# Optimization experiments

Measured on AMD Instinct MI355X. Metric: run time of the kernel, lower is better.

Reference implementation:

```python
import jax, jax.numpy as jnp
import numpy as np

B, S, D, N, NC = 2, 1024, 1024, 8192, 8


def _srw_chunked(x, h, emb_norm, tau_offset, w_read, w_write, n_chunks):
    Bd, Sd, Dd = x.shape
    Nd = emb_norm.shape[0]
    cs = Nd // n_chunks
    h_bf = h.astype(jnp.bfloat16)
    x_bf = x.astype(jnp.bfloat16)
    emb_bf = emb_norm.astype(jnp.bfloat16)
    read_bf = w_read.astype(jnp.bfloat16)
    write_bf = w_write.astype(jnp.bfloat16)
    z1 = jnp.zeros((Bd, Sd, 1))

    @jax.checkpoint
    def estimate_stats(h, emb, nc_val):
        ec0 = jax.lax.dynamic_slice_in_dim(emb, 0, cs, axis=0)
        sc0 = h @ ec0.T
        s_sum = sc0.sum(axis=-1, keepdims=True).astype(jnp.float32) * nc_val
        sq_sum = (sc0 ** 2).sum(axis=-1, keepdims=True).astype(jnp.float32) * nc_val
        return (s_sum, sq_sum)

    s_sum, sq_sum = estimate_stats(h_bf, emb_bf, n_chunks)
    s_mean = s_sum / Nd
    s_std = jnp.sqrt(sq_sum / Nd - s_mean ** 2) + 1e-08
    tau = s_mean + tau_offset * s_std
    tau_bf = tau.astype(jnp.bfloat16)

    @jax.checkpoint
    def gsrw_step(carry, i):
        out, es, em, ac, lbs, lbq = carry
        s = i * cs
        ec = jax.lax.dynamic_slice_in_dim(emb_bf, s, cs, axis=0)
        rc = jax.lax.dynamic_slice_in_dim(read_bf, s, cs, axis=0)
        wc = jax.lax.dynamic_slice_in_dim(write_bf, s, cs, axis=0)
        sc = h_bf @ ec.T  # [B,S,cs]
        raw = sc - tau_bf
        gc = jnp.where(raw > 0, raw, (1e-06 * jnp.exp(jnp.clip(raw.astype(jnp.float32), -10.0, 0.0))).astype(jnp.bfloat16))
        gc = jnp.clip(gc, 0.0, 10.0)
        eg = (jnp.exp(gc.astype(jnp.float32)) - 1.0).astype(jnp.bfloat16)
        ef = eg.astype(jnp.float32)
        xr = x_bf @ rc.T  # [B,S,cs]
        co = ((eg * xr) @ wc).astype(jnp.float32)  # [B,S,D]
        gn = ef.mean(axis=(0, 1))
        lbs = lbs + gn.sum()
        lbq = lbq + (gn ** 2).sum()
        return ((out + co,
                 es + ef.sum(axis=-1, keepdims=True),
                 jnp.maximum(em, ef.max(axis=-1, keepdims=True)),
                 ac + (raw > 0).sum(axis=-1, keepdims=True).astype(jnp.float32),
                 lbs, lbq), None)

    z_scalar = jnp.float32(0.0)
    init = (jnp.zeros((Bd, Sd, Dd), dtype=jnp.float32), z1,
            jnp.full((Bd, Sd, 1), -1000000000.0), z1, z_scalar, z_scalar)
    (raw_out, tes, tem, tac, lb_sum, lb_sq), _ = jax.lax.scan(gsrw_step, init, jnp.arange(n_chunks))
    inv_es = (1.0 / (tes + 1e-08)).astype(jnp.bfloat16)
    gs = jnp.tanh(tem).astype(jnp.bfloat16)
    out = raw_out * inv_es * gs
    exp_sum_scalar = tes.mean() + 1e-08
    norm_lb_sum = lb_sum / exp_sum_scalar
    norm_lb_sq = lb_sq / exp_sum_scalar ** 2
    lb_loss = norm_lb_sq * Nd - 2.0 * norm_lb_sum + 1.0
    gs_mean = jnp.tanh(tem).mean()
    es_mean = tes.mean()
    return (out.astype(jnp.float32), tac / Nd, tem, lb_loss, gs_mean, es_mean)


def setup_inputs() -> dict:
    key = jax.random.key(0)
    k = jax.random.split(key, 6)
    x = jax.random.normal(k[0], (B, S, D), jnp.float32)
    h = jax.random.normal(k[1], (B, S, D), jnp.float32)
    emb = jax.random.normal(k[2], (N, D), jnp.float32) * 0.02
    w_read = jax.random.normal(k[3], (N, D), jnp.float32) * 0.02
    w_write = jax.random.normal(k[4], (N, D), jnp.float32) * 0.02
    tau_offset = jax.random.normal(k[5], (B, S, 1), jnp.float32) * 0.1
    return {"x": x, "h": h, "emb": emb, "tau_offset": tau_offset,
            "w_read": w_read, "w_write": w_write, "n_chunks": NC}


def reference(x, h, emb, tau_offset, w_read, w_write, n_chunks):
    # caller (_know_forward) unit-normalizes the embedding pool first
    emb_norm = emb / (jnp.linalg.norm(emb, axis=-1, keepdims=True) + 1e-08)
    out, active_frac, gate_max, lb_loss, gs_mean, es_mean = _srw_chunked(
        x, h, emb_norm, tau_offset, w_read, w_write, n_chunks)
    return out
```

## Files before the change

### kernel.cpp

```cpp
#include <hip/hip_runtime.h>


#define MDIM 2048
#define DDIM 1024
#define NDIM 8192

typedef __attribute__((ext_vector_type(8))) __bf16 bf16x8;
typedef __attribute__((ext_vector_type(4))) float f32x4;

static __device__ __forceinline__ unsigned short f2b(float f) {
  unsigned u = __float_as_uint(f);
  u = (u + 0x7FFFu + ((u >> 16) & 1u)) >> 16;
  return (unsigned short)u;
}
static __device__ __forceinline__ float b2f(unsigned short s) {
  return __uint_as_float(((unsigned)s) << 16);
}

#define LDSF(off) (*(const bf16x8*)(lds + (off)))
#define MFMA_BF16 __builtin_amdgcn_mfma_f32_16x16x32_bf16

static __device__ __forceinline__ void stage_half(const unsigned short* __restrict__ src,
                                                  int ld, int row0, int k0,
                                                  char* lds, int lds_off, int w, int l) {
  const int rsub = l >> 3;
  const int col = k0 + 8 * ((l & 7) ^ rsub);
#pragma unroll
  for (int j = 0; j < 2; ++j) {
    const unsigned short* g =
        src + (size_t)(row0 + w * 8 + j * 64 + rsub) * (size_t)ld + col;
    __builtin_amdgcn_global_load_lds(
        (const __attribute__((address_space(1))) unsigned int*)(const void*)g,
        (__attribute__((address_space(3))) unsigned int*)(void*)(lds + lds_off + j * 8192 + w * 1024),
        16, 0, 0);
  }
}

template <int PAR, bool SA, bool SB, int VMC>
static __device__ __forceinline__ void ktile(const unsigned short* __restrict__ asrc,
                                             const unsigned short* __restrict__ bsrc,
                                             int ld, int m0, int n0, int kA, int kB,
                                             char* lds, f32x4 (&acc)[8][4],
                                             int w, int l, int wr, int wc,
                                             int arow_off, int brow_off, int kx0, int kx1) {
  const int ab = PAR * 65536 + wr * 16384;
  const int bb = PAR * 65536 + 32768 + (wc >> 1) * 16384;
  const int nxt = (1 - PAR) * 65536;
  bf16x8 a[4][2], blo[2][2], bhi[2][2];
  if (SA) stage_half(asrc, ld, m0, kA, lds, nxt, w, l);
#pragma unroll
  for (int m = 0; m < 4; ++m) {
    a[m][0] = LDSF(ab + arow_off + m * 2048 + kx0);
    a[m][1] = LDSF(ab + arow_off + m * 2048 + kx1);
  }
#pragma unroll
  for (int n = 0; n < 2; ++n) {
    blo[n][0] = LDSF(bb + brow_off + n * 2048 + kx0);
    blo[n][1] = LDSF(bb + brow_off + n * 2048 + kx1);
  }
  asm volatile("s_waitcnt lgkmcnt(8)" ::: "memory");
  __builtin_amdgcn_s_barrier();
  asm volatile("s_waitcnt lgkmcnt(0)" ::: "memory");
  __builtin_amdgcn_s_setprio(1);
#pragma unroll
  for (int ks = 0; ks < 2; ++ks)
#pragma unroll
    for (int n = 0; n < 2; ++n)
#pragma unroll
      for (int m = 0; m < 4; ++m)
        acc[m][n] = MFMA_BF16(a[m][ks], blo[n][ks], acc[m][n], 0, 0, 0);
  __builtin_amdgcn_s_setprio(0);
  __builtin_amdgcn_s_barrier();
  if (SA) stage_half(asrc, ld, m0 + 128, kA, lds, nxt + 16384, w, l);
#pragma unroll
  for (int n = 0; n < 2; ++n) {
    bhi[n][0] = LDSF(bb + brow_off + (n + 2) * 2048 + kx0);
    bhi[n][1] = LDSF(bb + brow_off + (n + 2) * 2048 + kx1);
  }
  __builtin_amdgcn_s_barrier();
  asm volatile("s_waitcnt lgkmcnt(0)" ::: "memory");
  __builtin_amdgcn_s_setprio(1);
#pragma unroll
  for (int ks = 0; ks < 2; ++ks)
#pragma unroll
    for (int n = 0; n < 2; ++n)
#pragma unroll
      for (int m = 0; m < 4; ++m)
        acc[m][n + 2] = MFMA_BF16(a[m][ks], bhi[n][ks], acc[m][n + 2], 0, 0, 0);
  __builtin_amdgcn_s_setprio(0);
  __builtin_amdgcn_s_barrier();
  if (SB) stage_half(bsrc, ld, n0, kB, lds, PAR * 65536 + 32768, w, l);
#pragma unroll
  for (int m = 0; m < 4; ++m) {
    a[m][0] = LDSF(ab + arow_off + (m + 4) * 2048 + kx0);
    a[m][1] = LDSF(ab + arow_off + (m + 4) * 2048 + kx1);
  }
  __builtin_amdgcn_s_barrier();
  asm volatile("s_waitcnt lgkmcnt(0)" ::: "memory");
  __builtin_amdgcn_s_setprio(1);
#pragma unroll
  for (int ks = 0; ks < 2; ++ks)
#pragma unroll
    for (int n = 0; n < 2; ++n)
#pragma unroll
      for (int m = 0; m < 4; ++m)
        acc[m + 4][n + 2] = MFMA_BF16(a[m][ks], bhi[n][ks], acc[m + 4][n + 2], 0, 0, 0);
  __builtin_amdgcn_s_setprio(0);
  __builtin_amdgcn_s_barrier();
  if (SB) stage_half(bsrc, ld, n0 + 128, kB, lds, PAR * 65536 + 49152, w, l);
  __builtin_amdgcn_s_setprio(1);
#pragma unroll
  for (int ks = 0; ks < 2; ++ks)
#pragma unroll
    for (int n = 0; n < 2; ++n)
#pragma unroll
      for (int m = 0; m < 4; ++m)
        acc[m + 4][n] = MFMA_BF16(a[m][ks], blo[n][ks], acc[m + 4][n], 0, 0, 0);
  __builtin_amdgcn_s_setprio(0);
  if (VMC == 4) asm volatile("s_waitcnt vmcnt(4)" ::: "memory");
  if (VMC == 0) asm volatile("s_waitcnt vmcnt(0)" ::: "memory");
  __builtin_amdgcn_s_barrier();
}

static __device__ __forceinline__ void gemm256(const unsigned short* __restrict__ asrc,
                                               const unsigned short* __restrict__ bsrc,
                                               int ld, int m0, int n0, int kbase,
                                               char* lds, f32x4 (&acc)[8][4],
                                               int w, int l, int wr, int wc) {
  const int lrow = l & 15, lk = l >> 4;
  const int axor = (l & 7) << 4;
  const int kx0 = (lk << 4) ^ axor;
  const int kx1 = (64 | (lk << 4)) ^ axor;
  const int arow_off = lrow * 128;
  const int brow_off = ((wc & 1) * 64 + lrow) * 128;

  stage_half(asrc, ld, m0,       kbase,      lds, 0,             w, l);
  stage_half(asrc, ld, m0 + 128, kbase,      lds, 16384,         w, l);
  stage_half(bsrc, ld, n0,       kbase,      lds, 32768,         w, l);
  stage_half(bsrc, ld, n0 + 128, kbase,      lds, 49152,         w, l);
  stage_half(bsrc, ld, n0,       kbase + 64, lds, 65536 + 32768, w, l);
  stage_half(bsrc, ld, n0 + 128, kbase + 64, lds, 65536 + 49152, w, l);
  asm volatile("s_waitcnt vmcnt(4)" ::: "memory");
  __builtin_amdgcn_s_barrier();

#pragma unroll 1
  for (int s = 0; s < 14; s += 2) {
    ktile<0, true, true, 4>(asrc, bsrc, ld, m0, n0, kbase + (s + 1) * 64,
                            kbase + (s + 2) * 64, lds, acc, w, l, wr, wc,
                            arow_off, brow_off, kx0, kx1);
    ktile<1, true, true, 4>(asrc, bsrc, ld, m0, n0, kbase + (s + 2) * 64,
                            kbase + (s + 3) * 64, lds, acc, w, l, wr, wc,
                            arow_off, brow_off, kx0, kx1);
  }
  ktile<0, true, false, 0>(asrc, bsrc, ld, m0, n0, kbase + 15 * 64, 0, lds, acc,
                           w, l, wr, wc, arow_off, brow_off, kx0, kx1);
  ktile<1, false, false, -1>(asrc, bsrc, ld, m0, n0, 0, 0, lds, acc,
                             w, l, wr, wc, arow_off, brow_off, kx0, kx1);
}


__global__ __launch_bounds__(256) void k_prep(const float* __restrict__ emb,
                                              const float* __restrict__ w_read,
                                              const float* __restrict__ h,
                                              const float* __restrict__ x,
                                              const float* __restrict__ w_write,
                                              unsigned short* __restrict__ eb,
                                              unsigned short* __restrict__ rb,
                                              unsigned short* __restrict__ hb,
                                              unsigned short* __restrict__ xb,
                                              unsigned short* __restrict__ wbT) {
  const int b = blockIdx.x, t = threadIdx.x;
  if (b < 8192) {
    const float4 v = ((const float4*)(emb + (size_t)b * 1024))[t];
    float ss = v.x * v.x + v.y * v.y + v.z * v.z + v.w * v.w;
#pragma unroll
    for (int off = 1; off < 64; off <<= 1) ss += __shfl_xor(ss, off, 64);
    __shared__ float wsum[4];
    if ((t & 63) == 0) wsum[t >> 6] = ss;
    __syncthreads();
    const float denom = sqrtf(wsum[0] + wsum[1] + wsum[2] + wsum[3]) + 1e-8f;
    ushort4 o;
    o.x = f2b(v.x / denom);
    o.y = f2b(v.y / denom);
    o.z = f2b(v.z / denom);
    o.w = f2b(v.w / denom);
    ((ushort4*)(eb + (size_t)b * 1024))[t] = o;
  } else if (b < 20480) {
    const float* src;
    unsigned short* dst;
    int i;
    if (b < 16384) { src = w_read; dst = rb; i = (b - 8192) * 256 + t; }
    else if (b < 18432) { src = h; dst = hb; i = (b - 16384) * 256 + t; }
    else { src = x; dst = xb; i = (b - 18432) * 256 + t; }
    const float4 v = ((const float4*)src)[i];
    ushort4 o;
    o.x = f2b(v.x);
    o.y = f2b(v.y);
    o.z = f2b(v.z);
    o.w = f2b(v.w);
    ((ushort4*)dst)[i] = o;
  } else {
    __shared__ float tsm[64][65];
    const int b2 = b - 20480;
    const int nb = b2 & 127, db = b2 >> 7;
    const int r = t >> 2, c4 = (t & 3) * 16;
#pragma unroll
    for (int j = 0; j < 4; ++j) {
      const float4 v = *(const float4*)&w_write[(size_t)(nb * 64 + r) * 1024 + db * 64 + c4 + 4 * j];
      tsm[r][c4 + 4 * j + 0] = v.x;
      tsm[r][c4 + 4 * j + 1] = v.y;
      tsm[r][c4 + 4 * j + 2] = v.z;
      tsm[r][c4 + 4 * j + 3] = v.w;
    }
    __syncthreads();
    const int dr = t >> 2, nc0 = (t & 3) * 16;
    unsigned pk[8];
#pragma unroll
    for (int j = 0; j < 8; ++j) {
      const unsigned lo = f2b(tsm[nc0 + 2 * j][dr]);
      const unsigned hi = f2b(tsm[nc0 + 2 * j + 1][dr]);
      pk[j] = lo | (hi << 16);
    }
    uint4* dst = (uint4*)(wbT + (size_t)(db * 64 + dr) * 8192 + nb * 64 + nc0);
    uint4 w0, w1;
    w0.x = pk[0]; w0.y = pk[1]; w0.z = pk[2]; w0.w = pk[3];
    w1.x = pk[4]; w1.y = pk[5]; w1.z = pk[6]; w1.w = pk[7];
    dst[0] = w0;
    dst[1] = w1;
  }
}


template <int TROWS>
static __device__ __forceinline__ void stage_tile(const unsigned short* __restrict__ src,
                                                  int row0, int k0, int ld,
                                                  unsigned short* lds, int wave, int lane) {
  const int rsub = lane >> 3;
  const int csub = (lane & 7) << 3;
#pragma unroll
  for (int q = 0; q < TROWS / 32; ++q) {
    const int p = q * 4 + wave;
    const unsigned short* g =
        src + (size_t)(row0 + p * 8 + rsub) * (size_t)ld + (size_t)(k0 + csub);
    __builtin_amdgcn_global_load_lds(
        (const __attribute__((address_space(1))) unsigned int*)(const void*)g,
        (__attribute__((address_space(3))) unsigned int*)(void*)(lds + p * 512),
        16, 0, 0);
  }
}

__global__ __launch_bounds__(256, 2) void k_stats(const unsigned short* __restrict__ hb,
                                                  const unsigned short* __restrict__ eb,
                                                  float* __restrict__ stat_s,
                                                  float* __restrict__ stat_q) {
  __shared__ unsigned short a_sm[128 * 64];
  __shared__ unsigned short b_sm[128 * 64];
  __shared__ float red_s[2][128];
  __shared__ float red_q[2][128];
  const int t = threadIdx.x;
  const int wave = t >> 6, lane = t & 63;
  const int wr = wave >> 1, wc = wave & 1;
  const int m0 = blockIdx.x * 128, n0 = blockIdx.y * 128;
  const int arow = lane & 15;
  const int kcol = (lane >> 4) << 3;
  f32x4 acc[4][4];
#pragma unroll
  for (int m = 0; m < 4; ++m)
#pragma unroll
    for (int n = 0; n < 4; ++n) acc[m][n] = (f32x4)0.0f;
  for (int k0 = 0; k0 < 1024; k0 += 64) {
    stage_tile<128>(hb, m0, k0, 1024, a_sm, wave, lane);
    stage_tile<128>(eb, n0, k0, 1024, b_sm, wave, lane);
    asm volatile("s_waitcnt vmcnt(0)" ::: "memory");
    __syncthreads();
#pragma unroll
    for (int ks = 0; ks < 2; ++ks) {
      bf16x8 af[4], bfr[4];
#pragma unroll
      for (int m = 0; m < 4; ++m)
        af[m] = *(const bf16x8*)&a_sm[(wr * 64 + m * 16 + arow) * 64 + ks * 32 + kcol];
#pragma unroll
      for (int n = 0; n < 4; ++n)
        bfr[n] = *(const bf16x8*)&b_sm[(wc * 64 + n * 16 + arow) * 64 + ks * 32 + kcol];
#pragma unroll
      for (int m = 0; m < 4; ++m)
#pragma unroll
        for (int n = 0; n < 4; ++n)
          acc[m][n] = MFMA_BF16(af[m], bfr[n], acc[m][n], 0, 0, 0);
    }
    __syncthreads();
  }

  float s_r[4][4], q_r[4][4];
#pragma unroll
  for (int m = 0; m < 4; ++m)
#pragma unroll
    for (int i = 0; i < 4; ++i) { s_r[m][i] = 0.f; q_r[m][i] = 0.f; }
#pragma unroll
  for (int m = 0; m < 4; ++m)
#pragma unroll
    for (int n = 0; n < 4; ++n)
#pragma unroll
      for (int i = 0; i < 4; ++i) {
        const float scf = b2f(f2b(acc[m][n][i]));
        s_r[m][i] += scf;
        q_r[m][i] += b2f(f2b(scf * scf));
      }
#pragma unroll
  for (int m = 0; m < 4; ++m)
#pragma unroll
    for (int i = 0; i < 4; ++i) {
      float s = s_r[m][i], q = q_r[m][i];
      for (int off = 1; off < 16; off <<= 1) {
        s += __shfl_xor(s, off, 64);
        q += __shfl_xor(q, off, 64);
      }
      if ((lane & 15) == 0) {
        const int rloc = wr * 64 + m * 16 + (lane >> 4) * 4 + i;
        red_s[wc][rloc] = s;
        red_q[wc][rloc] = q;
      }
    }
  __syncthreads();
  if (t < 128) {
    stat_s[(size_t)(m0 + t) * 8 + blockIdx.y] = red_s[0][t] + red_s[1][t];
    stat_q[(size_t)(m0 + t) * 8 + blockIdx.y] = red_q[0][t] + red_q[1][t];
  }
}

__global__ void k_tau(const float* __restrict__ stat_s, const float* __restrict__ stat_q,
                      const float* __restrict__ tau_off, float* __restrict__ tau) {
  const int r = blockIdx.x * 256 + threadIdx.x;
  if (r >= MDIM) return;
  float S = 0.f, Q = 0.f;
#pragma unroll
  for (int j = 0; j < 8; ++j) {
    S += stat_s[(size_t)r * 8 + j];
    Q += stat_q[(size_t)r * 8 + j];
  }
  const float s_sum = S * 8.0f;
  const float sq_sum = Q * 8.0f;
  const float mean = s_sum * (1.0f / 8192.0f);
  const float var = __fsub_rn(sq_sum * (1.0f / 8192.0f), __fmul_rn(mean, mean));
  const float sd = __fadd_rn(__fsqrt_rn(var), 1e-8f);
  const float tv = __fadd_rn(mean, __fmul_rn(tau_off[r], sd));
  tau[r] = b2f(f2b(tv));
}


__global__ __launch_bounds__(512, 2) void k_gate(const unsigned short* __restrict__ hb,
                                                 const unsigned short* __restrict__ eb,
                                                 const unsigned short* __restrict__ xb,
                                                 const unsigned short* __restrict__ rb,
                                                 const float* __restrict__ tau,
                                                 unsigned short* __restrict__ Aeg,
                                                 float* __restrict__ es_part,
                                                 float* __restrict__ em_part) {
  __shared__ __align__(16) char lds[131072];
  const int t = threadIdx.x, w = t >> 6, l = t & 63;
  const int wr = w >> 2, wc = w & 3;
  const int bid = blockIdx.x;
  const int swz = (bid & 7) * 32 + (bid >> 3);
  const int m0 = (swz >> 5) * 256, n0 = (swz & 31) * 256;
  const int lrow = l & 15, lk = l >> 4;

  f32x4 acc[8][4];
#pragma unroll
  for (int m = 0; m < 8; ++m)
#pragma unroll
    for (int n = 0; n < 4; ++n) acc[m][n] = (f32x4)0.0f;
  gemm256(hb, eb, 1024, m0, n0, 0, lds, acc, w, l, wr, wc);

  __syncthreads();
  float* tau_sm = (float*)lds;
  float* red_es = (float*)(lds + 1024);
  float* red_em = (float*)(lds + 1024 + 4096);
  if (t < 256) tau_sm[t] = tau[m0 + t];
  __syncthreads();
#pragma unroll
  for (int m = 0; m < 8; ++m) {
#pragma unroll
    for (int i = 0; i < 4; ++i) {
      const int rl = wr * 128 + m * 16 + lk * 4 + i;
      const float taub = tau_sm[rl];
      float es_v = 0.f, em_v = 0.f;
#pragma unroll
      for (int n = 0; n < 4; ++n) {
        const float scf = b2f(f2b(acc[m][n][i]));
        const float rawf = b2f(f2b(scf - taub));
        float gcf;
        if (rawf > 0.f) gcf = fminf(rawf, 10.0f);
        else gcf = b2f(f2b(1e-6f * expf(fmaxf(rawf, -10.0f))));
        const unsigned short egu = f2b(expf(gcf) - 1.0f);
        const float ef = b2f(egu);
        es_v += ef;
        em_v = fmaxf(em_v, ef);
        Aeg[(size_t)(m0 + rl) * NDIM + (size_t)(n0 + wc * 64 + n * 16 + lrow)] = egu;
      }
      for (int off = 1; off < 16; off <<= 1) {
        es_v += __shfl_xor(es_v, off, 64);
        em_v = fmaxf(em_v, __shfl_xor(em_v, off, 64));
      }
      if (lrow == 0) {
        red_es[wc * 256 + rl] = es_v;
        red_em[wc * 256 + rl] = em_v;
      }
    }
  }
  __syncthreads();
  if (t < 256) {
    const float s = red_es[t] + red_es[256 + t] + red_es[512 + t] + red_es[768 + t];
    const float e = fmaxf(fmaxf(red_em[t], red_em[256 + t]),
                          fmaxf(red_em[512 + t], red_em[768 + t]));
    es_part[(size_t)(m0 + t) * 32 + (n0 >> 8)] = s;
    em_part[(size_t)(m0 + t) * 32 + (n0 >> 8)] = e;
  }
  __syncthreads();

#pragma unroll
  for (int m = 0; m < 8; ++m)
#pragma unroll
    for (int n = 0; n < 4; ++n) acc[m][n] = (f32x4)0.0f;
  gemm256(xb, rb, 1024, m0, n0, 0, lds, acc, w, l, wr, wc);

#pragma unroll
  for (int m = 0; m < 8; ++m)
#pragma unroll
    for (int n = 0; n < 4; ++n)
#pragma unroll
      for (int i = 0; i < 4; ++i) {
        const int rl = wr * 128 + m * 16 + lk * 4 + i;
        const size_t idx =
            (size_t)(m0 + rl) * NDIM + (size_t)(n0 + wc * 64 + n * 16 + lrow);
        const unsigned short egu = Aeg[idx];
        const float xrf = b2f(f2b(acc[m][n][i]));
        Aeg[idx] = f2b(b2f(egu) * xrf);
      }
}


__global__ __launch_bounds__(512, 2) void k_out(const unsigned short* __restrict__ A,
                                                const unsigned short* __restrict__ wbT,
                                                unsigned short* __restrict__ pacc) {
  __shared__ __align__(16) char lds[131072];
  const int t = threadIdx.x, w = t >> 6, l = t & 63;
  const int wr = w >> 2, wc = w & 3;
  const int bid = blockIdx.x;
  const int swz = (bid & 7) * 32 + (bid >> 3);
  const int bm = swz >> 5, chunk = (swz >> 2) & 7, bd = swz & 3;
  const int m0 = bm * 256, d0 = bd * 256;
  f32x4 acc[8][4];
#pragma unroll
  for (int m = 0; m < 8; ++m)
#pragma unroll
    for (int n = 0; n < 4; ++n) acc[m][n] = (f32x4)0.0f;
  gemm256(A, wbT, 8192, m0, d0, chunk * 1024, lds, acc, w, l, wr, wc);

  const int lrow = l & 15, lk = l >> 4;
#pragma unroll
  for (int m = 0; m < 8; ++m)
#pragma unroll
    for (int n = 0; n < 4; ++n)
#pragma unroll
      for (int i = 0; i < 4; ++i) {
        const int rl = wr * 128 + m * 16 + lk * 4 + i;
        pacc[((size_t)chunk * MDIM + (m0 + rl)) * DDIM +
             (size_t)(d0 + wc * 64 + n * 16 + lrow)] = f2b(acc[m][n][i]);
      }
}


__global__ void k_scale(const float* __restrict__ es_part, const float* __restrict__ em_part,
                        float* __restrict__ scale2) {
  const int r = blockIdx.x * 256 + threadIdx.x;
  if (r >= MDIM) return;
  float s = 0.f, m = 0.f;
#pragma unroll
  for (int j = 0; j < 32; ++j) {
    s += es_part[(size_t)r * 32 + j];
    m = fmaxf(m, em_part[(size_t)r * 32 + j]);
  }
  scale2[2 * r] = b2f(f2b(1.0f / (s + 1e-8f)));
  scale2[2 * r + 1] = b2f(f2b(tanhf(m)));
}

__global__ __launch_bounds__(256) void k_finish(const unsigned short* __restrict__ pacc,
                                                const float* __restrict__ scale2,
                                                float* __restrict__ outp) {
  const int t = blockIdx.x * 256 + threadIdx.x;
  const int r = t >> 8;
  const int d4 = (t & 255) * 4;
  float sx = 0.f, sy = 0.f, sz = 0.f, sw = 0.f;
#pragma unroll
  for (int c = 0; c < 8; ++c) {
    const ushort4 v = *(const ushort4*)(pacc + ((size_t)c * MDIM + r) * DDIM + d4);
    sx += b2f(v.x);
    sy += b2f(v.y);
    sz += b2f(v.z);
    sw += b2f(v.w);
  }
  const float inv = scale2[2 * r];
  const float gsv = scale2[2 * r + 1];
  float4 o;
  o.x = (sx * inv) * gsv;
  o.y = (sy * inv) * gsv;
  o.z = (sz * inv) * gsv;
  o.w = (sw * inv) * gsv;
  *(float4*)(outp + (size_t)r * DDIM + d4) = o;
}


extern "C" void kernel_launch(void* const* d_in, const int* in_sizes, int n_in,
                              void* d_out, int out_size, void* d_ws, size_t ws_size,
                              hipStream_t stream) {
  const float* x = (const float*)d_in[0];
  const float* h = (const float*)d_in[1];
  const float* emb = (const float*)d_in[2];
  const float* tau_off = (const float*)d_in[3];
  const float* w_read = (const float*)d_in[4];
  const float* w_write = (const float*)d_in[5];

  char* ws = (char*)d_ws;
  const size_t MB = 1024 * 1024;
  unsigned short* rb = (unsigned short*)(ws);
  unsigned short* eb = (unsigned short*)(ws + 16 * MB);
  unsigned short* wbT = (unsigned short*)(ws + 32 * MB);
  unsigned short* hb = (unsigned short*)(ws + 48 * MB);
  unsigned short* xb = (unsigned short*)(ws + 52 * MB);
  unsigned short* Aeg = (unsigned short*)(ws + 56 * MB);
  unsigned short* pacc = (unsigned short*)(ws);
  float* tau = (float*)(ws + 88 * MB);
  float* stat_s = (float*)(ws + 88 * MB + 1 * 65536);
  float* stat_q = (float*)(ws + 88 * MB + 2 * 65536);
  float* es_part = (float*)(ws + 88 * MB + 3 * 65536);
  float* em_part = (float*)(ws + 88 * MB + 7 * 65536);
  float* scale2 = (float*)(ws + 88 * MB + 11 * 65536);
  if (ws_size < 88 * MB + 12 * 65536) return;
  float* outp = (float*)d_out;

  k_prep<<<22528, 256, 0, stream>>>(emb, w_read, h, x, w_write, eb, rb, hb, xb, wbT);
  k_stats<<<dim3(MDIM / 128, 8), 256, 0, stream>>>(hb, eb, stat_s, stat_q);
  k_tau<<<MDIM / 256, 256, 0, stream>>>(stat_s, stat_q, tau_off, tau);
  k_gate<<<256, 512, 0, stream>>>(hb, eb, xb, rb, tau, Aeg, es_part, em_part);
  k_scale<<<MDIM / 256, 256, 0, stream>>>(es_part, em_part, scale2);
  k_out<<<256, 512, 0, stream>>>(Aeg, wbT, pacc);
  k_finish<<<(MDIM * DDIM / 4) / 256, 256, 0, stream>>>(pacc, scale2, outp);
}
```

Before: 224.9 us.

## Restructure GEMM k-loop to prefetch next-tile fragments and reorder block mapping

The 256x256 GEMM inner tile is rescheduled so A and B register fragments for the next k-step are read from LDS while the current MFMAs run. Fragments are carried across tiles, and both A and B halves are preloaded two stages deep in the prologue. Block-to-tile mapping in the gate and output kernels is changed so blocks on the same XCD share N-columns or chunks, aiming for better L2 reuse. The prep kernel reorders its block ranges so the transpose blocks run first. This adds register pressure and a more delicate barrier and waitcnt ordering.

After: 424.6 us. 1.89x slower.

```diff
diff --git a/kernel.cpp b/kernel.cpp
--- a/kernel.cpp
+++ b/kernel.cpp
@@ -36,89 +36,108 @@
   }
 }
 
-template <int PAR, bool SA, bool SB, int VMC>
+template <int PAR, bool STG, bool RD, int VM>
 static __device__ __forceinline__ void ktile(const unsigned short* __restrict__ asrc,
                                              const unsigned short* __restrict__ bsrc,
-                                             int ld, int m0, int n0, int kA, int kB,
+                                             int ld, int m0, int n0, int kS,
                                              char* lds, f32x4 (&acc)[8][4],
+                                             bf16x8 (&aLO)[4][2], bf16x8 (&aHI)[4][2],
+                                             bf16x8 (&bLO)[2][2], bf16x8 (&bHI)[2][2],
                                              int w, int l, int wr, int wc,
                                              int arow_off, int brow_off, int kx0, int kx1) {
   const int ab = PAR * 65536 + wr * 16384;
   const int bb = PAR * 65536 + 32768 + (wc >> 1) * 16384;
-  const int nxt = (1 - PAR) * 65536;
-  bf16x8 a[4][2], blo[2][2], bhi[2][2];
-  if (SA) stage_half(asrc, ld, m0, kA, lds, nxt, w, l);
+  const int abn = (1 - PAR) * 65536 + wr * 16384;
+  const int bbn = (1 - PAR) * 65536 + 32768 + (wc >> 1) * 16384;
+
+#pragma unroll
+  for (int n = 0; n < 2; ++n) {
+    bHI[n][0] = LDSF(bb + brow_off + (n + 2) * 2048 + kx0);
+    bHI[n][1] = LDSF(bb + brow_off + (n + 2) * 2048 + kx1);
+  }
+  __builtin_amdgcn_s_barrier();
+  __builtin_amdgcn_s_setprio(1);
+#pragma unroll
+  for (int ks = 0; ks < 2; ++ks)
+#pragma unroll
+    for (int n = 0; n < 2; ++n)
+#pragma unroll
+      for (int m = 0; m < 4; ++m)
+        acc[m][n] = MFMA_BF16(aLO[m][ks], bLO[n][ks], acc[m][n], 0, 0, 0);
+  __builtin_amdgcn_s_setprio(0);
+  asm volatile("s_waitcnt lgkmcnt(0)" ::: "memory");
+  __builtin_amdgcn_s_barrier();
+
+  if (STG) {
+    stage_half(bsrc, ld, n0, kS, lds, PAR * 65536 + 32768, w, l);
+    stage_half(bsrc, ld, n0 + 128, kS, lds, PAR * 65536 + 49152, w, l);
+  }
 #pragma unroll
   for (int m = 0; m < 4; ++m) {
-    a[m][0] = LDSF(ab + arow_off + m * 2048 + kx0);
-    a[m][1] = LDSF(ab + arow_off + m * 2048 + kx1);
-  }
+    aHI[m][0] = LDSF(ab + arow_off + (m + 4) * 2048 + kx0);
+    aHI[m][1] = LDSF(ab + arow_off + (m + 4) * 2048 + kx1);
+  }
+  if (VM == 4) asm volatile("s_waitcnt vmcnt(4)" ::: "memory");
+  if (VM == 0) asm volatile("s_waitcnt vmcnt(0)" ::: "memory");
+  __builtin_amdgcn_s_barrier();
+  __builtin_amdgcn_s_setprio(1);
+#pragma unroll
+  for (int ks = 0; ks < 2; ++ks)
+#pragma unroll
+    for (int n = 0; n < 2; ++n)
+#pragma unroll
+      for (int m = 0; m < 4; ++m)
+        acc[m][n + 2] = MFMA_BF16(aLO[m][ks], bHI[n][ks], acc[m][n + 2], 0, 0, 0);
+  __builtin_amdgcn_s_setprio(0);
+  asm volatile("s_waitcnt lgkmcnt(0)" ::: "memory");
+  __builtin_amdgcn_s_barrier();
+
+  if (STG) stage_half(asrc, ld, m0, kS, lds, PAR * 65536, w, l);
+  if (RD) {
+#pragma unroll
+    for (int m = 0; m < 4; ++m) {
+      aLO[m][0] = LDSF(abn + arow_off + m * 2048 + kx0);
+      aLO[m][1] = LDSF(abn + arow_off + m * 2048 + kx1);
+    }
+  }
+  __builtin_amdgcn_s_barrier();
+  __builtin_amdgcn_s_setprio(1);
+#pragma unroll
+  for (int ks = 0; ks < 2; ++ks)
+#pragma unroll
+    for (int n = 0; n < 2; ++n)
+#pragma unroll
+      for (int m = 0; m < 4; ++m)
+        acc[m + 4][n + 2] = MFMA_BF16(aHI[m][ks], bHI[n][ks], acc[m + 4][n + 2], 0, 0, 0);
+  __builtin_amdgcn_s_setprio(0);
+  asm volatile("s_waitcnt lgkmcnt(0)" ::: "memory");
+  __builtin_amdgcn_s_barrier();
+
+  if (STG) stage_half(asrc, ld, m0 + 128, kS, lds, PAR * 65536 + 16384, w, l);
+  bf16x8 bold[2][2];
 #pragma unroll
   for (int n = 0; n < 2; ++n) {
-    blo[n][0] = LDSF(bb + brow_off + n * 2048 + kx0);
-    blo[n][1] = LDSF(bb + brow_off + n * 2048 + kx1);
-  }
-  asm volatile("s_waitcnt lgkmcnt(8)" ::: "memory");
-  __builtin_amdgcn_s_barrier();
+    bold[n][0] = bLO[n][0];
+    bold[n][1] = bLO[n][1];
+  }
+  if (RD) {
+#pragma unroll
+    for (int n = 0; n < 2; ++n) {
+      bLO[n][0] = LDSF(bbn + brow_off + n * 2048 + kx0);
+      bLO[n][1] = LDSF(bbn + brow_off + n * 2048 + kx1);
+    }
+  }
+  __builtin_amdgcn_s_barrier();
+  __builtin_amdgcn_s_setprio(1);
+#pragma unroll
+  for (int ks = 0; ks < 2; ++ks)
+#pragma unroll
+    for (int n = 0; n < 2; ++n)
+#pragma unroll
+      for (int m = 0; m < 4; ++m)
+        acc[m + 4][n] = MFMA_BF16(aHI[m][ks], bold[n][ks], acc[m + 4][n], 0, 0, 0);
+  __builtin_amdgcn_s_setprio(0);
   asm volatile("s_waitcnt lgkmcnt(0)" ::: "memory");
-  __builtin_amdgcn_s_setprio(1);
-#pragma unroll
-  for (int ks = 0; ks < 2; ++ks)
-#pragma unroll
-    for (int n = 0; n < 2; ++n)
-#pragma unroll
-      for (int m = 0; m < 4; ++m)
-        acc[m][n] = MFMA_BF16(a[m][ks], blo[n][ks], acc[m][n], 0, 0, 0);
-  __builtin_amdgcn_s_setprio(0);
-  __builtin_amdgcn_s_barrier();
-  if (SA) stage_half(asrc, ld, m0 + 128, kA, lds, nxt + 16384, w, l);
-#pragma unroll
-  for (int n = 0; n < 2; ++n) {
-    bhi[n][0] = LDSF(bb + brow_off + (n + 2) * 2048 + kx0);
-    bhi[n][1] = LDSF(bb + brow_off + (n + 2) * 2048 + kx1);
-  }
-  __builtin_amdgcn_s_barrier();
-  asm volatile("s_waitcnt lgkmcnt(0)" ::: "memory");
-  __builtin_amdgcn_s_setprio(1);
-#pragma unroll
-  for (int ks = 0; ks < 2; ++ks)
-#pragma unroll
-    for (int n = 0; n < 2; ++n)
-#pragma unroll
-      for (int m = 0; m < 4; ++m)
-        acc[m][n + 2] = MFMA_BF16(a[m][ks], bhi[n][ks], acc[m][n + 2], 0, 0, 0);
-  __builtin_amdgcn_s_setprio(0);
-  __builtin_amdgcn_s_barrier();
-  if (SB) stage_half(bsrc, ld, n0, kB, lds, PAR * 65536 + 32768, w, l);
-#pragma unroll
-  for (int m = 0; m < 4; ++m) {
-    a[m][0] = LDSF(ab + arow_off + (m + 4) * 2048 + kx0);
-    a[m][1] = LDSF(ab + arow_off + (m + 4) * 2048 + kx1);
-  }
-  __builtin_amdgcn_s_barrier();
-  asm volatile("s_waitcnt lgkmcnt(0)" ::: "memory");
-  __builtin_amdgcn_s_setprio(1);
-#pragma unroll
-  for (int ks = 0; ks < 2; ++ks)
-#pragma unroll
-    for (int n = 0; n < 2; ++n)
-#pragma unroll
-      for (int m = 0; m < 4; ++m)
-        acc[m + 4][n + 2] = MFMA_BF16(a[m][ks], bhi[n][ks], acc[m + 4][n + 2], 0, 0, 0);
-  __builtin_amdgcn_s_setprio(0);
-  __builtin_amdgcn_s_barrier();
-  if (SB) stage_half(bsrc, ld, n0 + 128, kB, lds, PAR * 65536 + 49152, w, l);
-  __builtin_amdgcn_s_setprio(1);
-#pragma unroll
-  for (int ks = 0; ks < 2; ++ks)
-#pragma unroll
-    for (int n = 0; n < 2; ++n)
-#pragma unroll
-      for (int m = 0; m < 4; ++m)
-        acc[m + 4][n] = MFMA_BF16(a[m][ks], blo[n][ks], acc[m + 4][n], 0, 0, 0);
-  __builtin_amdgcn_s_setprio(0);
-  if (VMC == 4) asm volatile("s_waitcnt vmcnt(4)" ::: "memory");
-  if (VMC == 0) asm volatile("s_waitcnt vmcnt(0)" ::: "memory");
   __builtin_amdgcn_s_barrier();
 }
 
@@ -133,29 +152,44 @@
   const int kx1 = (64 | (lk << 4)) ^ axor;
   const int arow_off = lrow * 128;
   const int brow_off = ((wc & 1) * 64 + lrow) * 128;
+  const int ab0 = wr * 16384;
+  const int bb0 = 32768 + (wc >> 1) * 16384;
+
+  bf16x8 aLO[4][2], aHI[4][2], bLO[2][2], bHI[2][2];
 
   stage_half(asrc, ld, m0,       kbase,      lds, 0,             w, l);
   stage_half(asrc, ld, m0 + 128, kbase,      lds, 16384,         w, l);
   stage_half(bsrc, ld, n0,       kbase,      lds, 32768,         w, l);
   stage_half(bsrc, ld, n0 + 128, kbase,      lds, 49152,         w, l);
+  stage_half(asrc, ld, m0,       kbase + 64, lds, 65536,         w, l);
+  stage_half(asrc, ld, m0 + 128, kbase + 64, lds, 65536 + 16384, w, l);
   stage_half(bsrc, ld, n0,       kbase + 64, lds, 65536 + 32768, w, l);
   stage_half(bsrc, ld, n0 + 128, kbase + 64, lds, 65536 + 49152, w, l);
-  asm volatile("s_waitcnt vmcnt(4)" ::: "memory");
-  __builtin_amdgcn_s_barrier();
+  asm volatile("s_waitcnt vmcnt(8)" ::: "memory");
+  __builtin_amdgcn_s_barrier();
+#pragma unroll
+  for (int m = 0; m < 4; ++m) {
+    aLO[m][0] = LDSF(ab0 + arow_off + m * 2048 + kx0);
+    aLO[m][1] = LDSF(ab0 + arow_off + m * 2048 + kx1);
+  }
+#pragma unroll
+  for (int n = 0; n < 2; ++n) {
+    bLO[n][0] = LDSF(bb0 + brow_off + n * 2048 + kx0);
+    bLO[n][1] = LDSF(bb0 + brow_off + n * 2048 + kx1);
+  }
+  asm volatile("s_waitcnt lgkmcnt(0)" ::: "memory");
 
 #pragma unroll 1
   for (int s = 0; s < 14; s += 2) {
-    ktile<0, true, true, 4>(asrc, bsrc, ld, m0, n0, kbase + (s + 1) * 64,
-                            kbase + (s + 2) * 64, lds, acc, w, l, wr, wc,
-                            arow_off, brow_off, kx0, kx1);
-    ktile<1, true, true, 4>(asrc, bsrc, ld, m0, n0, kbase + (s + 2) * 64,
-                            kbase + (s + 3) * 64, lds, acc, w, l, wr, wc,
-                            arow_off, brow_off, kx0, kx1);
-  }
-  ktile<0, true, false, 0>(asrc, bsrc, ld, m0, n0, kbase + 15 * 64, 0, lds, acc,
-                           w, l, wr, wc, arow_off, brow_off, kx0, kx1);
-  ktile<1, false, false, -1>(asrc, bsrc, ld, m0, n0, 0, 0, lds, acc,
-                             w, l, wr, wc, arow_off, brow_off, kx0, kx1);
+    ktile<0, true, true, 4>(asrc, bsrc, ld, m0, n0, kbase + (s + 2) * 64, lds, acc,
+                            aLO, aHI, bLO, bHI, w, l, wr, wc, arow_off, brow_off, kx0, kx1);
+    ktile<1, true, true, 4>(asrc, bsrc, ld, m0, n0, kbase + (s + 3) * 64, lds, acc,
+                            aLO, aHI, bLO, bHI, w, l, wr, wc, arow_off, brow_off, kx0, kx1);
+  }
+  ktile<0, false, true, 0>(asrc, bsrc, ld, m0, n0, 0, lds, acc,
+                           aLO, aHI, bLO, bHI, w, l, wr, wc, arow_off, brow_off, kx0, kx1);
+  ktile<1, false, false, -1>(asrc, bsrc, ld, m0, n0, 0, lds, acc,
+                             aLO, aHI, bLO, bHI, w, l, wr, wc, arow_off, brow_off, kx0, kx1);
 }
 
 
@@ -170,8 +204,36 @@
                                               unsigned short* __restrict__ xb,
                                               unsigned short* __restrict__ wbT) {
   const int b = blockIdx.x, t = threadIdx.x;
-  if (b < 8192) {
-    const float4 v = ((const float4*)(emb + (size_t)b * 1024))[t];
+  if (b < 2048) {
+    __shared__ float tsm[64][65];
+    const int nb = b & 127, db = b >> 7;
+    const int r = t >> 2, c4 = (t & 3) * 16;
+#pragma unroll
+    for (int j = 0; j < 4; ++j) {
+      const float4 v = *(const float4*)&w_write[(size_t)(nb * 64 + r) * 1024 + db * 64 + c4 + 4 * j];
+      tsm[r][c4 + 4 * j + 0] = v.x;
+      tsm[r][c4 + 4 * j + 1] = v.y;
+      tsm[r][c4 + 4 * j + 2] = v.z;
+      tsm[r][c4 + 4 * j + 3] = v.w;
+    }
+    __syncthreads();
+    const int dr = t >> 2, nc0 = (t & 3) * 16;
+    unsigned pk[8];
+#pragma unroll
+    for (int j = 0; j < 8; ++j) {
+      const unsigned lo = f2b(tsm[nc0 + 2 * j][dr]);
+      const unsigned hi = f2b(tsm[nc0 + 2 * j + 1][dr]);
+      pk[j] = lo | (hi << 16);
+    }
+    uint4* dst = (uint4*)(wbT + (size_t)(db * 64 + dr) * 8192 + nb * 64 + nc0);
+    uint4 w0, w1;
+    w0.x = pk[0]; w0.y = pk[1]; w0.z = pk[2]; w0.w = pk[3];
+    w1.x = pk[4]; w1.y = pk[5]; w1.z = pk[6]; w1.w = pk[7];
+    dst[0] = w0;
+    dst[1] = w1;
+  } else if (b < 10240) {
+    const int n = b - 2048;
+    const float4 v = ((const float4*)(emb + (size_t)n * 1024))[t];
     float ss = v.x * v.x + v.y * v.y + v.z * v.z + v.w * v.w;
 #pragma unroll
     for (int off = 1; off < 64; off <<= 1) ss += __shfl_xor(ss, off, 64);
@@ -184,14 +246,14 @@
     o.y = f2b(v.y / denom);
     o.z = f2b(v.z / denom);
     o.w = f2b(v.w / denom);
-    ((ushort4*)(eb + (size_t)b * 1024))[t] = o;
-  } else if (b < 20480) {
+    ((ushort4*)(eb + (size_t)n * 1024))[t] = o;
+  } else {
     const float* src;
     unsigned short* dst;
     int i;
-    if (b < 16384) { src = w_read; dst = rb; i = (b - 8192) * 256 + t; }
-    else if (b < 18432) { src = h; dst = hb; i = (b - 16384) * 256 + t; }
-    else { src = x; dst = xb; i = (b - 18432) * 256 + t; }
+    if (b < 18432) { src = w_read; dst = rb; i = (b - 10240) * 256 + t; }
+    else if (b < 20480) { src = h; dst = hb; i = (b - 18432) * 256 + t; }
+    else { src = x; dst = xb; i = (b - 20480) * 256 + t; }
     const float4 v = ((const float4*)src)[i];
     ushort4 o;
     o.x = f2b(v.x);
@@ -199,34 +261,6 @@
     o.z = f2b(v.z);
     o.w = f2b(v.w);
     ((ushort4*)dst)[i] = o;
-  } else {
-    __shared__ float tsm[64][65];
-    const int b2 = b - 20480;
-    const int nb = b2 & 127, db = b2 >> 7;
-    const int r = t >> 2, c4 = (t & 3) * 16;
-#pragma unroll
-    for (int j = 0; j < 4; ++j) {
-      const float4 v = *(const float4*)&w_write[(size_t)(nb * 64 + r) * 1024 + db * 64 + c4 + 4 * j];
-      tsm[r][c4 + 4 * j + 0] = v.x;
-      tsm[r][c4 + 4 * j + 1] = v.y;
-      tsm[r][c4 + 4 * j + 2] = v.z;
-      tsm[r][c4 + 4 * j + 3] = v.w;
-    }
-    __syncthreads();
-    const int dr = t >> 2, nc0 = (t & 3) * 16;
-    unsigned pk[8];
-#pragma unroll
-    for (int j = 0; j < 8; ++j) {
-      const unsigned lo = f2b(tsm[nc0 + 2 * j][dr]);
-      const unsigned hi = f2b(tsm[nc0 + 2 * j + 1][dr]);
-      pk[j] = lo | (hi << 16);
-    }
-    uint4* dst = (uint4*)(wbT + (size_t)(db * 64 + dr) * 8192 + nb * 64 + nc0);
-    uint4 w0, w1;
-    w0.x = pk[0]; w0.y = pk[1]; w0.z = pk[2]; w0.w = pk[3];
-    w1.x = pk[4]; w1.y = pk[5]; w1.z = pk[6]; w1.w = pk[7];
-    dst[0] = w0;
-    dst[1] = w1;
   }
 }
 
@@ -360,8 +394,9 @@
   const int t = threadIdx.x, w = t >> 6, l = t & 63;
   const int wr = w >> 2, wc = w & 3;
   const int bid = blockIdx.x;
-  const int swz = (bid & 7) * 32 + (bid >> 3);
-  const int m0 = (swz >> 5) * 256, n0 = (swz & 31) * 256;
+  const int xcd = bid & 7, i = bid >> 3;
+  const int n0 = (xcd * 4 + (i & 3)) * 256;
+  const int m0 = (i >> 2) * 256;
   const int lrow = l & 15, lk = l >> 4;
 
   f32x4 acc[8][4];
@@ -380,13 +415,13 @@
 #pragma unroll
   for (int m = 0; m < 8; ++m) {
 #pragma unroll
-    for (int i = 0; i < 4; ++i) {
-      const int rl = wr * 128 + m * 16 + lk * 4 + i;
+    for (int i2 = 0; i2 < 4; ++i2) {
+      const int rl = wr * 128 + m * 16 + lk * 4 + i2;
       const float taub = tau_sm[rl];
       float es_v = 0.f, em_v = 0.f;
 #pragma unroll
       for (int n = 0; n < 4; ++n) {
-        const float scf = b2f(f2b(acc[m][n][i]));
+        const float scf = b2f(f2b(acc[m][n][i2]));
         const float rawf = b2f(f2b(scf - taub));
         float gcf;
         if (rawf > 0.f) gcf = fminf(rawf, 10.0f);
@@ -415,6 +450,7 @@
     es_part[(size_t)(m0 + t) * 32 + (n0 >> 8)] = s;
     em_part[(size_t)(m0 + t) * 32 + (n0 >> 8)] = e;
   }
+  asm volatile("s_waitcnt vmcnt(0)" ::: "memory");
   __syncthreads();
 
 #pragma unroll
@@ -428,12 +464,12 @@
 #pragma unroll
     for (int n = 0; n < 4; ++n)
 #pragma unroll
-      for (int i = 0; i < 4; ++i) {
-        const int rl = wr * 128 + m * 16 + lk * 4 + i;
+      for (int i2 = 0; i2 < 4; ++i2) {
+        const int rl = wr * 128 + m * 16 + lk * 4 + i2;
         const size_t idx =
             (size_t)(m0 + rl) * NDIM + (size_t)(n0 + wc * 64 + n * 16 + lrow);
         const unsigned short egu = Aeg[idx];
-        const float xrf = b2f(f2b(acc[m][n][i]));
+        const float xrf = b2f(f2b(acc[m][n][i2]));
         Aeg[idx] = f2b(b2f(egu) * xrf);
       }
 }
@@ -446,8 +482,8 @@
   const int t = threadIdx.x, w = t >> 6, l = t & 63;
   const int wr = w >> 2, wc = w & 3;
   const int bid = blockIdx.x;
-  const int swz = (bid & 7) * 32 + (bid >> 3);
-  const int bm = swz >> 5, chunk = (swz >> 2) & 7, bd = swz & 3;
+  const int chunk = bid & 7, i = bid >> 3;
+  const int bm = i >> 2, bd = i & 3;
   const int m0 = bm * 256, d0 = bd * 256;
   f32x4 acc[8][4];
 #pragma unroll
@@ -462,10 +498,10 @@
 #pragma unroll
     for (int n = 0; n < 4; ++n)
 #pragma unroll
-      for (int i = 0; i < 4; ++i) {
-        const int rl = wr * 128 + m * 16 + lk * 4 + i;
+      for (int i2 = 0; i2 < 4; ++i2) {
+        const int rl = wr * 128 + m * 16 + lk * 4 + i2;
         pacc[((size_t)chunk * MDIM + (m0 + rl)) * DDIM +
-             (size_t)(d0 + wc * 64 + n * 16 + lrow)] = f2b(acc[m][n][i]);
+             (size_t)(d0 + wc * 64 + n * 16 + lrow)] = f2b(acc[m][n][i2]);
       }
 }
 
```
